# Kernel optimization log

Hardware: AMD Instinct MI355X
Metric: run time of the kernel (lower is better)

## Reference

```python
import jax, jax.numpy as jnp
import numpy as np

N_HEADS = 16
N_QUBITS = 7
DIM = 2 ** N_QUBITS  # per-head state dimension = 128


def _rotation_gates(params):
    """params: [H, nq, 3] -> composite Rz@Ry@Rx gates [H, nq, 2, 2] complex64."""
    a = params[..., 0] / 2.0
    b = params[..., 1] / 2.0
    c = params[..., 2] / 2.0
    ca, sa = jnp.cos(a), jnp.sin(a)
    cb, sb = jnp.cos(b), jnp.sin(b)
    i_ = jnp.complex64(1j)
    rx = jnp.stack([jnp.stack([ca + 0j, -i_ * sa], -1),
                    jnp.stack([-i_ * sa, ca + 0j], -1)], -2)  # [H,nq,2,2]
    ry = jnp.stack([jnp.stack([cb + 0j, -sb + 0j], -1),
                    jnp.stack([sb + 0j, cb + 0j], -1)], -2)
    z = jnp.zeros_like(c) + 0j
    rz = jnp.stack([jnp.stack([jnp.exp(-i_ * c), z], -1),
                    jnp.stack([z, jnp.exp(i_ * c)], -1)], -2)
    return jnp.einsum('...ij,...jk,...kl->...il', rz, ry, rx).astype(jnp.complex64)


def _quantum_transform(states, params):
    """states: [B,S,H,D] real; params: [H,nq,3]. Apply per-qubit gates then measure |psi|^2.
    Qubit q acts on axis q of the state reshaped to [2]*n_qubits (q=0 most significant)."""
    B, S, H, D = states.shape
    gates = _rotation_gates(params)  # [H, nq, 2, 2]
    psi = states.astype(jnp.complex64)
    for q in range(N_QUBITS):
        L = 2 ** q
        R = D // (2 * L)
        psi = psi.reshape(B, S, H, L, 2, R)
        psi = jnp.einsum('hij,bshljr->bshlir', gates[:, q], psi)
        psi = psi.reshape(B, S, H, D)
    return psi.real ** 2 + psi.imag ** 2  # measurement probabilities, real fp32


def setup_inputs() -> dict:
    key = jax.random.key(0)
    ks = jax.random.split(key, 6)
    B, S = 2, 2048
    return {
        'states': jax.random.normal(ks[0], (B, S, N_HEADS * DIM), dtype=jnp.float32),
        'attention_mask': jnp.ones((B, S), dtype=jnp.int32),
        'query_params': jax.random.normal(ks[1], (N_HEADS, N_QUBITS, 3), dtype=jnp.float32),
        'key_params': jax.random.normal(ks[2], (N_HEADS, N_QUBITS, 3), dtype=jnp.float32),
        'value_params': jax.random.normal(ks[3], (N_HEADS, N_QUBITS, 3), dtype=jnp.float32),
        'W_out': jax.random.normal(ks[4], (DIM, N_HEADS * DIM), dtype=jnp.float32) / np.sqrt(N_HEADS * DIM),
        'b_out': jnp.zeros((DIM,), dtype=jnp.float32),
    }


def reference(states, attention_mask, query_params, key_params, value_params, W_out, b_out):
    B, S, F = states.shape
    x = states.reshape(B, S, N_HEADS, DIM)  # split heads
    q = _quantum_transform(x, query_params)   # [B,S,H,D]
    k = _quantum_transform(x, key_params)
    v = _quantum_transform(x, value_params)
    scores = jnp.einsum('bqhd,bkhd->bhqk', q, k) / np.sqrt(DIM)  # [B,H,S,S]
    mask = attention_mask[:, None, None, :] != 0  # [B,1,1,S]
    scores = jnp.where(mask, scores, jnp.float32(-jnp.inf))
    probs = jax.nn.softmax(scores, axis=-1)
    ctx = jnp.einsum('bhqk,bkhd->bqhd', probs, v)  # [B,S,H,D]
    concat = ctx.reshape(B, S, N_HEADS * DIM)
    return concat @ W_out.T + b_out  # [B,S,D]
```

## Files before the change

### kernel.cpp

```cpp
#include <hip/hip_runtime.h>
#include <math.h>

#define NH 16
#define DD 128
#define SS 2048
#define NQ 7

typedef __attribute__((ext_vector_type(8))) short bf16x8;
typedef __attribute__((ext_vector_type(16))) float f32x16;

#define MFMA32(a,b,c) __builtin_amdgcn_mfma_f32_32x32x16_bf16(a,b,c,0,0,0)

__device__ __forceinline__ unsigned pkbf(float a, float b){
    unsigned ua = __float_as_uint(a); ua += 0x7FFF + ((ua>>16)&1);
    unsigned ub = __float_as_uint(b); ub += 0x7FFF + ((ub>>16)&1);
    return (ua>>16) | (ub & 0xFFFF0000u);
}

__device__ __forceinline__ void gl_lds16(const int4* g, int4* l){
    __builtin_amdgcn_global_load_lds((const __attribute__((address_space(1))) void*)g,
                                     (__attribute__((address_space(3))) void*)l, 16, 0, 0);
}

struct cplx { float r, i; };
__device__ __forceinline__ cplx cmul(cplx a, cplx b){ cplx o; o.r = a.r*b.r - a.i*b.i; o.i = a.r*b.i + a.i*b.r; return o; }
__device__ __forceinline__ cplx cadd(cplx a, cplx b){ cplx o; o.r = a.r+b.r; o.i = a.i+b.i; return o; }

__global__ void gates_kernel(const float* __restrict__ qp, const float* __restrict__ kp,
                             const float* __restrict__ vp, float* __restrict__ gates){
    for (int it = threadIdx.x; it < 3*NH*NQ; it += 256){
        int set = it / (NH*NQ);
        int rem = it % (NH*NQ);
        const float* p = (set==0 ? qp : (set==1 ? kp : vp)) + rem*3;
        float a = p[0]*0.5f, b = p[1]*0.5f, c = p[2]*0.5f;
        float ca=cosf(a), sa=sinf(a), cb=cosf(b), sb=sinf(b), cc=cosf(c), sc=sinf(c);
        cplx rx00={ca,0.f}, rx01={0.f,-sa}, rx10={0.f,-sa}, rx11={ca,0.f};
        cplx ry00={cb,0.f}, ry01={-sb,0.f}, ry10={sb,0.f}, ry11={cb,0.f};
        cplx e0={cc,-sc}, e1={cc,sc};
        cplx m00 = cadd(cmul(ry00,rx00), cmul(ry01,rx10));
        cplx m01 = cadd(cmul(ry00,rx01), cmul(ry01,rx11));
        cplx m10 = cadd(cmul(ry10,rx00), cmul(ry11,rx10));
        cplx m11 = cadd(cmul(ry10,rx01), cmul(ry11,rx11));
        cplx g00 = cmul(e0,m00), g01 = cmul(e0,m01), g10 = cmul(e1,m10), g11 = cmul(e1,m11);
        float* gp = gates + it*8;
        gp[0]=g00.r; gp[1]=g00.i; gp[2]=g01.r; gp[3]=g01.i;
        gp[4]=g10.r; gp[5]=g10.i; gp[6]=g11.r; gp[7]=g11.i;
    }
}

__global__ __launch_bounds__(256) void prep2_kernel(const float* __restrict__ W,
        const float* __restrict__ gates, ushort* __restrict__ wfrag, ushort* __restrict__ ufrag){
    int t = threadIdx.x;
    if (blockIdx.x < 128){
        int tid = blockIdx.x*256 + t;
        int ln = tid & 31, hi = (tid>>5)&1, ds = (tid>>6)&127, ct = tid>>13;
        int n = ct*32 + ln;
        const float* src = W + (size_t)n*2048 + ds*16 + hi*8;
        float4 f0 = *(const float4*)(src);
        float4 f1 = *(const float4*)(src + 4);
        int4 o;
        o.x = (int)pkbf(f0.x, f0.y); o.y = (int)pkbf(f0.z, f0.w);
        o.z = (int)pkbf(f1.x, f1.y); o.w = (int)pkbf(f1.z, f1.w);
        ((int4*)wfrag)[tid] = o;
        return;
    }
    int sh = blockIdx.x - 128;
    const float* gp = gates + sh*NQ*8;
    float g[7][8];
    #pragma unroll
    for (int q=0;q<7;++q)
        #pragma unroll
        for (int e=0;e<8;++e) g[q][e] = gp[q*8+e];
    int4* uf = (int4*)ufrag;
    #pragma unroll
    for (int p=0;p<8;++p){
        int pos = t + p*256;
        int ln = pos & 31, hi = (pos>>5)&1, ds = (pos>>6)&7, ct = pos>>9;
        int dp = ct*32 + ln;
        int d0 = ds*16 + hi*8;
        cplx base = {1.f, 0.f};
        #pragma unroll
        for (int q=0;q<4;++q){
            int rb = (dp >> (6-q)) & 1, cb2 = (d0 >> (6-q)) & 1;
            cplx gv = { g[q][rb*4+cb2*2], g[q][rb*4+cb2*2+1] };
            base = cmul(base, gv);
        }
        int r4 = (dp>>2)&1, r5 = (dp>>1)&1, r6 = dp&1;
        float vr[8], vi[8];
        #pragma unroll
        for (int j=0;j<8;++j){
            cplx g4 = { g[4][r4*4 + ((j>>2)&1)*2], g[4][r4*4 + ((j>>2)&1)*2 + 1] };
            cplx g5 = { g[5][r5*4 + ((j>>1)&1)*2], g[5][r5*4 + ((j>>1)&1)*2 + 1] };
            cplx g6 = { g[6][r6*4 + (j&1)*2],      g[6][r6*4 + (j&1)*2 + 1] };
            cplx v = cmul(cmul(cmul(base, g4), g5), g6);
            vr[j] = v.r; vi[j] = v.i;
        }
        int4 outr, outi;
        outr.x = (int)pkbf(vr[0],vr[1]); outr.y = (int)pkbf(vr[2],vr[3]);
        outr.z = (int)pkbf(vr[4],vr[5]); outr.w = (int)pkbf(vr[6],vr[7]);
        outi.x = (int)pkbf(vi[0],vi[1]); outi.y = (int)pkbf(vi[2],vi[3]);
        outi.z = (int)pkbf(vi[4],vi[5]); outi.w = (int)pkbf(vi[6],vi[7]);
        uf[ ((sh*8 + ct)*8 + ds)*64 + hi*32 + ln ]     = outr;
        uf[ ((sh*8 + 4 + ct)*8 + ds)*64 + hi*32 + ln ] = outi;
    }
}

__global__ __launch_bounds__(256, 2) void qkv_kernel(const float* __restrict__ states,
        const ushort* __restrict__ ufrag, ushort* __restrict__ qfo,
        ushort* __restrict__ kfo, ushort* __restrict__ vfo){
    __shared__ int xs[128*66];
    int t = threadIdx.x, w = t>>6, lane = t&63, hi = lane>>5, ln = lane&31;
    int bh = blockIdx.x >> 4, stile = blockIdx.x & 15;
    int b = bh >> 4, h = bh & 15;
    int mt = stile*4 + w;
    const float sc = 0.08838834764831845f;
    {
        int tk = t >> 1, hf = t & 1;
        const float* src = states + ((size_t)(b*SS + stile*128 + tk))*2048 + h*128 + hf*64;
        int* dst = xs + tk*66 + hf*32;
        #pragma unroll
        for (int i=0;i<16;++i){
            float4 f = *(const float4*)(src + i*4);
            dst[i*2]   = (int)pkbf(f.x, f.y);
            dst[i*2+1] = (int)pkbf(f.z, f.w);
        }
    }
    __syncthreads();
    bf16x8 xf[8];
    #pragma unroll
    for (int ds=0; ds<8; ++ds){
        union { bf16x8 v; int2 d[2]; } c;
        const int2* base = (const int2*)(xs + (w*32 + ln)*66 + ds*8 + hi*4);
        c.d[0] = base[0]; c.d[1] = base[1];
        xf[ds] = c.v;
    }
    const int4* ub = (const int4*)ufrag;
    int4* qf4 = (int4*)qfo; int4* kf4 = (int4*)kfo; int4* vf4 = (int4*)vfo;
    #pragma unroll
    for (int set=0; set<3; ++set){
        int sh = set*16 + h;
        #pragma unroll
        for (int ct=0; ct<4; ++ct){
            bf16x8 ur[8], ui[8];
            #pragma unroll
            for (int ds=0; ds<8; ++ds){
                ur[ds] = *(const bf16x8*)(ub + ((sh*8 + ct)*8 + ds)*64 + lane);
                ui[ds] = *(const bf16x8*)(ub + ((sh*8 + 4 + ct)*8 + ds)*64 + lane);
            }
            f32x16 Cr, Ci;
            #pragma unroll
            for (int r=0;r<16;++r){ Cr[r]=0.f; Ci[r]=0.f; }
            if (set < 2){
                #pragma unroll
                for (int ds=0; ds<8; ++ds){
                    Cr = MFMA32(ur[ds], xf[ds], Cr);
                    Ci = MFMA32(ui[ds], xf[ds], Ci);
                }
            } else {
                #pragma unroll
                for (int ds=0; ds<8; ++ds){
                    Cr = MFMA32(xf[ds], ur[ds], Cr);
                    Ci = MFMA32(xf[ds], ui[ds], Ci);
                }
            }
            float pv[16];
            #pragma unroll
            for (int r=0;r<16;++r) pv[r] = Cr[r]*Cr[r] + Ci[r]*Ci[r];
            if (set == 0){
                #pragma unroll
                for (int r=0;r<16;++r) pv[r] *= sc;
            }
            unsigned u2[4][2];
            #pragma unroll
            for (int g2=0; g2<4; ++g2){
                u2[g2][0] = pkbf(pv[g2*4+0], pv[g2*4+1]);
                u2[g2][1] = pkbf(pv[g2*4+2], pv[g2*4+3]);
            }
            #pragma unroll
            for (int gg=0; gg<2; ++gg){
                int g2s = hi*2 + gg, g2p = g2s ^ 2;
                unsigned r0 = (unsigned)__shfl_xor((int)u2[g2p][0], 32);
                unsigned r1 = (unsigned)__shfl_xor((int)u2[g2p][1], 32);
                int4 frag;
                frag.x = (int)(hi ? r0 : u2[g2s][0]);
                frag.y = (int)(hi ? r1 : u2[g2s][1]);
                frag.z = (int)(hi ? u2[g2s][0] : r0);
                frag.w = (int)(hi ? u2[g2s][1] : r1);
                if (set == 0)
                    qf4[((bh*64 + mt)*8 + ct*2 + hi)*64 + gg*32 + ln] = frag;
                else if (set == 1)
                    kf4[((bh*64 + mt)*8 + ct*2 + hi)*64 + gg*32 + ln] = frag;
                else
                    vf4[((bh*4 + ct)*128 + mt*2 + hi)*64 + gg*32 + ln] = frag;
            }
        }
    }
}

__global__ __launch_bounds__(256, 2) void flash_kernel(const ushort* __restrict__ qfi,
        const ushort* __restrict__ kfi, const ushort* __restrict__ vfi,
        const int* __restrict__ mask, ushort* __restrict__ ctxf){
    __shared__ __align__(16) int4 kbuf[2][1024];
    __shared__ __align__(16) int4 vbuf[2][1024];
    int t = threadIdx.x, w = t>>6, lane = t&63, hi = lane>>5, ln = lane&31;
    int bh = blockIdx.x >> 4, qt = blockIdx.x & 15;
    int b = bh >> 4;
    const int4* qfp = (const int4*)qfi + (size_t)((bh*64 + qt*4 + w)*8)*64 + lane;
    bf16x8 qf[8];
    #pragma unroll
    for (int ds=0; ds<8; ++ds) qf[ds] = *(const bf16x8*)(qfp + ds*64);
    const int4* kg = (const int4*)kfi + (size_t)(bh*64*8)*64 + (w*4)*64 + lane;
    const int4* vg = (const int4*)vfi + ((size_t)(bh*4 + w)*128)*64 + lane;
    const int* mp = mask + b*SS;
    f32x16 O[4];
    #pragma unroll
    for (int d=0; d<4; ++d){
        #pragma unroll
        for (int r=0;r<16;++r) O[d][r] = 0.f;
    }
    float l = 0.f;
    {
        int4* kd = &kbuf[0][(w*4)*64];
        int4* vd = &vbuf[0][(w*4)*64];
        #pragma unroll
        for (int i=0;i<4;++i) gl_lds16(kg + i*64, kd + i*64);
        #pragma unroll
        for (int i=0;i<4;++i) gl_lds16(vg + i*64, vd + i*64);
    }
    for (int kt=0; kt<32; ++kt){
        int p = kt & 1;
        int mk = mp[kt*64 + lane];
        __syncthreads();
        if (kt < 31){
            int4* kd = &kbuf[p^1][(w*4)*64];
            int4* vd = &vbuf[p^1][(w*4)*64];
            const int4* ks = kg + (size_t)(kt+1)*1024;
            const int4* vs = vg + (kt+1)*4*64;
            #pragma unroll
            for (int i=0;i<4;++i) gl_lds16(ks + i*64, kd + i*64);
            #pragma unroll
            for (int i=0;i<4;++i) gl_lds16(vs + i*64, vd + i*64);
        }
        const int4* kl = kbuf[p];
        const int4* vl = vbuf[p];
        f32x16 S0, S1;
        #pragma unroll
        for (int r=0;r<16;++r){ S0[r]=0.f; S1[r]=0.f; }
        #pragma unroll
        for (int ds=0; ds<8; ++ds){
            bf16x8 k0 = *(const bf16x8*)(kl + ds*64 + lane);
            bf16x8 k1 = *(const bf16x8*)(kl + (8+ds)*64 + lane);
            S0 = MFMA32(k0, qf[ds], S0);
            S1 = MFMA32(k1, qf[ds], S1);
        }
        if (__ballot(mk != 0) != ~0ull){
            #pragma unroll
            for (int r=0;r<16;++r){
                int row0 = ((r>>2)<<3) + (hi<<2) + (r&3);
                if (__shfl(mk, row0) == 0)      S0[r] = -1e30f;
                if (__shfl(mk, 32 + row0) == 0) S1[r] = -1e30f;
            }
        }
        #pragma unroll
        for (int r=0;r<16;++r){
            S0[r] = __expf(S0[r] - 40.f); l += S0[r];
            S1[r] = __expf(S1[r] - 40.f); l += S1[r];
        }
        #pragma unroll
        for (int m2=0; m2<2; ++m2){
            #pragma unroll
            for (int T=0; T<2; ++T){
                const f32x16& P = m2 ? S1 : S0;
                unsigned A0 = pkbf(P[8*T+0], P[8*T+1]);
                unsigned A1 = pkbf(P[8*T+2], P[8*T+3]);
                unsigned B0 = pkbf(P[8*T+4], P[8*T+5]);
                unsigned B1 = pkbf(P[8*T+6], P[8*T+7]);
                unsigned X0 = hi ? A0 : B0, X1 = hi ? A1 : B1;
                unsigned Y0 = (unsigned)__shfl_xor((int)X0, 32);
                unsigned Y1 = (unsigned)__shfl_xor((int)X1, 32);
                union { bf16x8 v; unsigned u[4]; } pf;
                pf.u[0] = hi ? Y0 : A0;
                pf.u[1] = hi ? Y1 : A1;
                pf.u[2] = hi ? B0 : Y0;
                pf.u[3] = hi ? B1 : Y1;
                int tt = m2*2 + T;
                #pragma unroll
                for (int db=0; db<4; ++db){
                    bf16x8 vf = *(const bf16x8*)(vl + (db*4 + tt)*64 + lane);
                    O[db] = MFMA32(vf, pf.v, O[db]);
                }
            }
        }
    }
    l += __shfl_xor(l, 32);
    float inv = 1.f / l;
    int h = bh & 15;
    int mt = b*64 + qt*4 + w;
    int4* cf = (int4*)ctxf;
    #pragma unroll
    for (int db=0; db<4; ++db){
        unsigned u[4][2];
        #pragma unroll
        for (int g2=0; g2<4; ++g2){
            u[g2][0] = pkbf(O[db][g2*4+0]*inv, O[db][g2*4+1]*inv);
            u[g2][1] = pkbf(O[db][g2*4+2]*inv, O[db][g2*4+3]*inv);
        }
        #pragma unroll
        for (int gg=0; gg<2; ++gg){
            int g2s = hi*2 + gg;
            int g2p = g2s ^ 2;
            unsigned r0 = (unsigned)__shfl_xor((int)u[g2p][0], 32);
            unsigned r1 = (unsigned)__shfl_xor((int)u[g2p][1], 32);
            int4 frag;
            frag.x = (int)(hi ? r0 : u[g2s][0]);
            frag.y = (int)(hi ? r1 : u[g2s][1]);
            frag.z = (int)(hi ? u[g2s][0] : r0);
            frag.w = (int)(hi ? u[g2s][1] : r1);
            int ds = h*8 + db*2 + hi;
            cf[ ((size_t)(mt*128 + ds)*2 + gg)*32 + ln ] = frag;
        }
    }
}

__global__ __launch_bounds__(256) void proj_kernel(const ushort* __restrict__ ctxf,
                                                   const ushort* __restrict__ wfrag,
                                                   const float* __restrict__ bo,
                                                   float* __restrict__ out){
    int t = threadIdx.x, w = t >> 6, lane = t & 63;
    int hi = lane >> 5, ln = lane & 31;
    int mt = blockIdx.x, ct = w;
    const int4* A = (const int4*)ctxf + (size_t)mt*8192 + lane;
    const int4* B = (const int4*)wfrag + (size_t)ct*8192 + lane;
    f32x16 acc;
    #pragma unroll
    for (int r=0;r<16;++r) acc[r] = 0.f;
    #pragma unroll 8
    for (int ds=0; ds<128; ++ds){
        bf16x8 a = *(const bf16x8*)(A + (size_t)ds*64);
        bf16x8 b = *(const bf16x8*)(B + (size_t)ds*64);
        acc = MFMA32(a, b, acc);
    }
    float bias = bo[ct*32 + ln];
    float* op = out + (size_t)(mt*32)*128 + ct*32 + ln;
    #pragma unroll
    for (int r=0;r<16;++r){
        int row = (r&3) + 8*(r>>2) + 4*hi;
        op[(size_t)row*128] = acc[r] + bias;
    }
}

extern "C" void kernel_launch(void* const* d_in, const int* in_sizes, int n_in,
                              void* d_out, int out_size, void* d_ws, size_t ws_size,
                              hipStream_t stream){
    const float* states = (const float*)d_in[0];
    const int*   mask   = (const int*)d_in[1];
    const float* qp     = (const float*)d_in[2];
    const float* kp     = (const float*)d_in[3];
    const float* vp     = (const float*)d_in[4];
    const float* W      = (const float*)d_in[5];
    const float* bo     = (const float*)d_in[6];
    float* out = (float*)d_out;
    char* wsb = (char*)d_ws;
    float*  gates = (float*) wsb;
    ushort* wfrag = (ushort*)(wsb + 16384);
    ushort* ufrag = (ushort*)(wsb + 16384 + 524288);
    char*   big   = wsb + 16384 + 524288 + 3145728;
    ushort* qf    = (ushort*)(big);
    ushort* kf    = (ushort*)(big + 1u*16777216);
    ushort* vf    = (ushort*)(big + 2u*16777216);
    ushort* ctxf  = (ushort*)(big + 3u*16777216);
    hipLaunchKernelGGL(gates_kernel, dim3(1), dim3(256), 0, stream, qp, kp, vp, gates);
    hipLaunchKernelGGL(prep2_kernel, dim3(176), dim3(256), 0, stream, W, gates, wfrag, ufrag);
    hipLaunchKernelGGL(qkv_kernel, dim3(512), dim3(256), 0, stream, states, ufrag, qf, kf, vf);
    hipLaunchKernelGGL(flash_kernel, dim3(512), dim3(256), 0, stream, qf, kf, vf, mask, ctxf);
    hipLaunchKernelGGL(proj_kernel, dim3(128), dim3(256), 0, stream, ctxf, wfrag, bo, out);
}
```

Measured before the change: 232.3 us.

## Shrink flash KV tile, fold log2e into Q scale, use hardware bf16 convert

Several changes at once. The bf16 packing now uses the hardware cvt_pk_bf16_f32 builtin when it is available. The QKV kernel has each wave own one output column tile and loop over the token tiles, with coalesced loads of states and outer loops that are not unrolled. The flash kernel halves the KV tile to 32 keys, which halves shared memory and raises launch bounds to 4 blocks, and splits K and V staging across waves. It also folds log2(e) into the Q scale and the constant shift into the accumulator init, so it can use exp2f. More occupancy and less register pressure are traded for twice as many loop iterations and barriers. The fixed softmax shift constant could risk overflow or underflow.

```diff
diff --git a/kernel.cpp b/kernel.cpp
--- a/kernel.cpp
+++ b/kernel.cpp
@@ -12,9 +12,14 @@
 #define MFMA32(a,b,c) __builtin_amdgcn_mfma_f32_32x32x16_bf16(a,b,c,0,0,0)
 
 __device__ __forceinline__ unsigned pkbf(float a, float b){
+#if __has_builtin(__builtin_amdgcn_cvt_pk_bf16_f32)
+    auto v = __builtin_amdgcn_cvt_pk_bf16_f32(a, b);
+    unsigned u; __builtin_memcpy(&u, &v, 4); return u;
+#else
     unsigned ua = __float_as_uint(a); ua += 0x7FFF + ((ua>>16)&1);
     unsigned ub = __float_as_uint(b); ub += 0x7FFF + ((ub>>16)&1);
     return (ua>>16) | (ub & 0xFFFF0000u);
+#endif
 }
 
 __device__ __forceinline__ void gl_lds16(const int4* g, int4* l){
@@ -112,40 +117,40 @@
     int t = threadIdx.x, w = t>>6, lane = t&63, hi = lane>>5, ln = lane&31;
     int bh = blockIdx.x >> 4, stile = blockIdx.x & 15;
     int b = bh >> 4, h = bh & 15;
-    int mt = stile*4 + w;
-    const float sc = 0.08838834764831845f;
+    const float sc = 0.12751743f;
     {
-        int tk = t >> 1, hf = t & 1;
-        const float* src = states + ((size_t)(b*SS + stile*128 + tk))*2048 + h*128 + hf*64;
-        int* dst = xs + tk*66 + hf*32;
+        int c = t & 31, tk2 = t >> 5;
         #pragma unroll
         for (int i=0;i<16;++i){
-            float4 f = *(const float4*)(src + i*4);
-            dst[i*2]   = (int)pkbf(f.x, f.y);
-            dst[i*2+1] = (int)pkbf(f.z, f.w);
+            int tk = i*8 + tk2;
+            const float* src = states + ((size_t)(b*SS + stile*128 + tk))*2048 + h*128 + c*4;
+            float4 f = *(const float4*)src;
+            int2 o; o.x = (int)pkbf(f.x,f.y); o.y = (int)pkbf(f.z,f.w);
+            *(int2*)(xs + tk*66 + c*2) = o;
         }
     }
     __syncthreads();
-    bf16x8 xf[8];
-    #pragma unroll
-    for (int ds=0; ds<8; ++ds){
-        union { bf16x8 v; int2 d[2]; } c;
-        const int2* base = (const int2*)(xs + (w*32 + ln)*66 + ds*8 + hi*4);
-        c.d[0] = base[0]; c.d[1] = base[1];
-        xf[ds] = c.v;
-    }
+    int ct = w;
     const int4* ub = (const int4*)ufrag;
     int4* qf4 = (int4*)qfo; int4* kf4 = (int4*)kfo; int4* vf4 = (int4*)vfo;
-    #pragma unroll
+    #pragma unroll 1
     for (int set=0; set<3; ++set){
         int sh = set*16 + h;
-        #pragma unroll
-        for (int ct=0; ct<4; ++ct){
-            bf16x8 ur[8], ui[8];
+        bf16x8 ur[8], ui[8];
+        #pragma unroll
+        for (int ds=0; ds<8; ++ds){
+            ur[ds] = *(const bf16x8*)(ub + ((sh*8 + ct)*8 + ds)*64 + lane);
+            ui[ds] = *(const bf16x8*)(ub + ((sh*8 + 4 + ct)*8 + ds)*64 + lane);
+        }
+        #pragma unroll 1
+        for (int tt=0; tt<4; ++tt){
+            bf16x8 xf[8];
             #pragma unroll
             for (int ds=0; ds<8; ++ds){
-                ur[ds] = *(const bf16x8*)(ub + ((sh*8 + ct)*8 + ds)*64 + lane);
-                ui[ds] = *(const bf16x8*)(ub + ((sh*8 + 4 + ct)*8 + ds)*64 + lane);
+                union { bf16x8 v; int2 d[2]; } c;
+                const int2* base = (const int2*)(xs + (tt*32 + ln)*66 + ds*8 + hi*4);
+                c.d[0] = base[0]; c.d[1] = base[1];
+                xf[ds] = c.v;
             }
             f32x16 Cr, Ci;
             #pragma unroll
@@ -176,6 +181,7 @@
                 u2[g2][0] = pkbf(pv[g2*4+0], pv[g2*4+1]);
                 u2[g2][1] = pkbf(pv[g2*4+2], pv[g2*4+3]);
             }
+            int mt = stile*4 + tt;
             #pragma unroll
             for (int gg=0; gg<2; ++gg){
                 int g2s = hi*2 + gg, g2p = g2s ^ 2;
@@ -197,20 +203,21 @@
     }
 }
 
-__global__ __launch_bounds__(256, 2) void flash_kernel(const ushort* __restrict__ qfi,
+__global__ __launch_bounds__(256, 4) void flash_kernel(const ushort* __restrict__ qfi,
         const ushort* __restrict__ kfi, const ushort* __restrict__ vfi,
         const int* __restrict__ mask, ushort* __restrict__ ctxf){
-    __shared__ __align__(16) int4 kbuf[2][1024];
-    __shared__ __align__(16) int4 vbuf[2][1024];
+    __shared__ __align__(16) int4 kbuf[2][512];
+    __shared__ __align__(16) int4 vbuf[2][512];
     int t = threadIdx.x, w = t>>6, lane = t&63, hi = lane>>5, ln = lane&31;
     int bh = blockIdx.x >> 4, qt = blockIdx.x & 15;
     int b = bh >> 4;
+    const float NEGC = -57.7078018f;
     const int4* qfp = (const int4*)qfi + (size_t)((bh*64 + qt*4 + w)*8)*64 + lane;
     bf16x8 qf[8];
     #pragma unroll
     for (int ds=0; ds<8; ++ds) qf[ds] = *(const bf16x8*)(qfp + ds*64);
-    const int4* kg = (const int4*)kfi + (size_t)(bh*64*8)*64 + (w*4)*64 + lane;
-    const int4* vg = (const int4*)vfi + ((size_t)(bh*4 + w)*128)*64 + lane;
+    const int4* kroot = (const int4*)kfi + (size_t)(bh*64)*8*64 + lane;
+    const int4* vroot = (const int4*)vfi + (size_t)(bh*4)*128*64 + lane;
     const int* mp = mask + b*SS;
     f32x16 O[4];
     #pragma unroll
@@ -219,76 +226,66 @@
         for (int r=0;r<16;++r) O[d][r] = 0.f;
     }
     float l = 0.f;
-    {
-        int4* kd = &kbuf[0][(w*4)*64];
-        int4* vd = &vbuf[0][(w*4)*64];
-        #pragma unroll
-        for (int i=0;i<4;++i) gl_lds16(kg + i*64, kd + i*64);
-        #pragma unroll
-        for (int i=0;i<4;++i) gl_lds16(vg + i*64, vd + i*64);
-    }
-    for (int kt=0; kt<32; ++kt){
+    auto stage = [&](int kt, int pb){
+        if (w < 2){
+            int dsb = w*4;
+            const int4* src = kroot + ((size_t)kt*8 + dsb)*64;
+            int4* dst = &kbuf[pb][dsb*64];
+            #pragma unroll
+            for (int j=0;j<4;++j) gl_lds16(src + j*64, dst + j*64);
+        } else {
+            #pragma unroll
+            for (int j=0;j<4;++j){
+                int v = (w-2)*4 + j;
+                int db = v>>1, tt = v&1;
+                const int4* src = vroot + ((size_t)db*128 + kt*2 + tt)*64;
+                gl_lds16(src, &vbuf[pb][v*64]);
+            }
+        }
+    };
+    stage(0, 0);
+    for (int kt=0; kt<64; ++kt){
         int p = kt & 1;
-        int mk = mp[kt*64 + lane];
+        int mk = mp[kt*32 + ln];
         __syncthreads();
-        if (kt < 31){
-            int4* kd = &kbuf[p^1][(w*4)*64];
-            int4* vd = &vbuf[p^1][(w*4)*64];
-            const int4* ks = kg + (size_t)(kt+1)*1024;
-            const int4* vs = vg + (kt+1)*4*64;
-            #pragma unroll
-            for (int i=0;i<4;++i) gl_lds16(ks + i*64, kd + i*64);
-            #pragma unroll
-            for (int i=0;i<4;++i) gl_lds16(vs + i*64, vd + i*64);
-        }
+        if (kt < 63) stage(kt+1, p^1);
         const int4* kl = kbuf[p];
         const int4* vl = vbuf[p];
-        f32x16 S0, S1;
-        #pragma unroll
-        for (int r=0;r<16;++r){ S0[r]=0.f; S1[r]=0.f; }
+        f32x16 S;
+        #pragma unroll
+        for (int r=0;r<16;++r) S[r] = NEGC;
         #pragma unroll
         for (int ds=0; ds<8; ++ds){
-            bf16x8 k0 = *(const bf16x8*)(kl + ds*64 + lane);
-            bf16x8 k1 = *(const bf16x8*)(kl + (8+ds)*64 + lane);
-            S0 = MFMA32(k0, qf[ds], S0);
-            S1 = MFMA32(k1, qf[ds], S1);
+            bf16x8 kk = *(const bf16x8*)(kl + ds*64 + lane);
+            S = MFMA32(kk, qf[ds], S);
         }
         if (__ballot(mk != 0) != ~0ull){
             #pragma unroll
             for (int r=0;r<16;++r){
                 int row0 = ((r>>2)<<3) + (hi<<2) + (r&3);
-                if (__shfl(mk, row0) == 0)      S0[r] = -1e30f;
-                if (__shfl(mk, 32 + row0) == 0) S1[r] = -1e30f;
-            }
-        }
-        #pragma unroll
-        for (int r=0;r<16;++r){
-            S0[r] = __expf(S0[r] - 40.f); l += S0[r];
-            S1[r] = __expf(S1[r] - 40.f); l += S1[r];
-        }
-        #pragma unroll
-        for (int m2=0; m2<2; ++m2){
-            #pragma unroll
-            for (int T=0; T<2; ++T){
-                const f32x16& P = m2 ? S1 : S0;
-                unsigned A0 = pkbf(P[8*T+0], P[8*T+1]);
-                unsigned A1 = pkbf(P[8*T+2], P[8*T+3]);
-                unsigned B0 = pkbf(P[8*T+4], P[8*T+5]);
-                unsigned B1 = pkbf(P[8*T+6], P[8*T+7]);
-                unsigned X0 = hi ? A0 : B0, X1 = hi ? A1 : B1;
-                unsigned Y0 = (unsigned)__shfl_xor((int)X0, 32);
-                unsigned Y1 = (unsigned)__shfl_xor((int)X1, 32);
-                union { bf16x8 v; unsigned u[4]; } pf;
-                pf.u[0] = hi ? Y0 : A0;
-                pf.u[1] = hi ? Y1 : A1;
-                pf.u[2] = hi ? B0 : Y0;
-                pf.u[3] = hi ? B1 : Y1;
-                int tt = m2*2 + T;
-                #pragma unroll
-                for (int db=0; db<4; ++db){
-                    bf16x8 vf = *(const bf16x8*)(vl + (db*4 + tt)*64 + lane);
-                    O[db] = MFMA32(vf, pf.v, O[db]);
-                }
+                if (__shfl(mk, row0) == 0) S[r] = -1e30f;
+            }
+        }
+        #pragma unroll
+        for (int r=0;r<16;++r){ S[r] = exp2f(S[r]); l += S[r]; }
+        #pragma unroll
+        for (int T=0; T<2; ++T){
+            unsigned A0 = pkbf(S[8*T+0], S[8*T+1]);
+            unsigned A1 = pkbf(S[8*T+2], S[8*T+3]);
+            unsigned B0 = pkbf(S[8*T+4], S[8*T+5]);
+            unsigned B1 = pkbf(S[8*T+6], S[8*T+7]);
+            unsigned X0 = hi ? A0 : B0, X1 = hi ? A1 : B1;
+            unsigned Y0 = (unsigned)__shfl_xor((int)X0, 32);
+            unsigned Y1 = (unsigned)__shfl_xor((int)X1, 32);
+            union { bf16x8 v; unsigned u[4]; } pf;
+            pf.u[0] = hi ? Y0 : A0;
+            pf.u[1] = hi ? Y1 : A1;
+            pf.u[2] = hi ? B0 : Y0;
+            pf.u[3] = hi ? B1 : Y1;
+            #pragma unroll
+            for (int db=0; db<4; ++db){
+                bf16x8 vf = *(const bf16x8*)(vl + (db*2 + T)*64 + lane);
+                O[db] = MFMA32(vf, pf.v, O[db]);
             }
         }
     }
```

Measured after the change: 328.7 us. 41.5% more time.
